# Kernel tuning notes

Hardware: AMD Instinct MI355X
Metric: run time of the kernel (lower is better)

The kernel has to match this reference:

```python
import jax, jax.numpy as jnp
import numpy as np

PATCH = 3          # patch size for SSD cost
PAD = PATCH // 2
K_NN = 8           # number of NN candidates kept per pixel
N_ITERS = 10       # PatchMatch iterations (forward default n_iters=10)
_DY = jnp.array([d // PATCH for d in range(PATCH * PATCH)], dtype=jnp.int32)
_DX = jnp.array([d % PATCH for d in range(PATCH * PATCH)], dtype=jnp.int32)


def _patches(x):
    # x: [C,H,W] -> [C, P*P, H, W] edge-padded patch neighborhoods
    C, H, W = x.shape
    xp = jnp.pad(x, ((0, 0), (PAD, PAD), (PAD, PAD)), mode='edge')
    return jnp.stack([xp[:, dy:dy + H, dx:dx + W]
                      for dy in range(PATCH) for dx in range(PATCH)], axis=1)


def _cost(a_pat, b_pad, s):
    # a_pat: [C,P2,H,W]; b_pad: [C,H+2p,W+2p]; s: [2,H,W] int -> SSD cost [H,W]
    iy = s[0][None] + _DY[:, None, None]   # [P2,H,W]
    ix = s[1][None] + _DX[:, None, None]
    b_g = b_pad[:, iy, ix]                 # [C,P2,H,W] gathered target patches
    return jnp.sum((a_pat - b_g) ** 2, axis=(0, 1))


def patchmatch_search(a, b, key, k=K_NN, n_iters=N_ITERS):
    # a, b: [C,H,W]. Returns shifts [k,2,H,W] int32 and costs [k,H,W].
    C, H, W = a.shape
    a_pat = _patches(a)
    b_pad = jnp.pad(b, ((0, 0), (PAD, PAD), (PAD, PAD)), mode='edge')
    cost1 = lambda s: _cost(a_pat, b_pad, s)
    hi = jnp.array([H, W], dtype=jnp.int32).reshape(1, 2, 1, 1)
    dx1 = jnp.array([0, 1], jnp.int32).reshape(1, 2, 1, 1)
    dy1 = jnp.array([1, 0], jnp.int32).reshape(1, 2, 1, 1)
    k0, key = jax.random.split(key)
    shifts = jax.random.randint(k0, (k, 2, H, W), 0, hi)
    costs = jax.lax.map(cost1, shifts)
    radii = [max(W // 2, 1), max(W // 8, 1), max(W // 32, 1), 1]

    def step(carry, it):
        shifts, costs = carry
        kk = jax.random.fold_in(key, it)
        # parallel propagation of neighbors' shifts
        left = jnp.roll(shifts, 1, axis=3) + dx1
        right = jnp.roll(shifts, -1, axis=3) - dx1
        up = jnp.roll(shifts, 1, axis=2) + dy1
        down = jnp.roll(shifts, -1, axis=2) - dy1
        # random search with shrinking radii
        rand_c = [shifts + jax.random.randint(jax.random.fold_in(kk, i),
                                              shifts.shape, -r, r + 1)
                  for i, r in enumerate(radii)]
        cands = jnp.concatenate([left, right, up, down] + rand_c, axis=0)
        cands = jnp.clip(cands, 0, hi - 1)
        new_costs = jax.lax.map(cost1, cands)
        all_s = jnp.concatenate([shifts, cands], axis=0)      # [M,2,H,W]
        all_c = jnp.concatenate([costs, new_costs], axis=0)   # [M,H,W]
        neg_top, idx = jax.lax.top_k(-jnp.moveaxis(all_c, 0, -1), k)  # [H,W,k]
        s_hw = jnp.transpose(all_s, (2, 3, 0, 1))             # [H,W,M,2]
        sel = jnp.take_along_axis(s_hw, idx[..., None], axis=2)  # [H,W,k,2]
        return (jnp.transpose(sel, (2, 3, 0, 1)), jnp.moveaxis(-neg_top, -1, 0)), None

    (shifts, costs), _ = jax.lax.scan(step, (shifts, costs), jnp.arange(n_iters))
    return shifts, costs


def setup_inputs() -> dict:
    key = jax.random.key(0)
    kq, kk, kv = jax.random.split(key, 3)
    q = jax.random.normal(kq, (1, 32, 128, 128), jnp.float32)
    k = jax.random.normal(kk, (1, 32, 128, 128), jnp.float32)
    v = jax.random.normal(kv, (4, 64, 128, 128), jnp.float32)
    return {"q": q, "k": k, "v": v}


def reference(q, k, v):
    # PatchMatch k-NN search between q[0] and k[0]
    shifts, costs = patchmatch_search(q[0], k[0], jax.random.key(42))
    w = jax.nn.softmax(-costs, axis=0)                 # [K,H,W]
    g = v[:, :, shifts[:, 0], shifts[:, 1]]            # [B,Cv,K,H,W] gather
    return jnp.sum(w[None, None] * g, axis=2)          # [B,Cv,H,W]
```

## Files before the change

kernel.cpp:

```cpp
#include <hip/hip_runtime.h>
#include <cstdint>

#define NPIX 16384
#define KNN 8
#define PW 130
#define NPPAD (PW * PW)
#define NPH 8

typedef float f32x4 __attribute__((ext_vector_type(4)));
typedef __attribute__((address_space(3))) uint32_t lds_u32_t;
typedef const __attribute__((address_space(1))) uint32_t glob_u32_t;

__host__ __device__ __forceinline__ void tf2x32(uint32_t k0, uint32_t k1,
                                                uint32_t x0, uint32_t x1,
                                                uint32_t& o0, uint32_t& o1) {
  uint32_t ks2 = k0 ^ k1 ^ 0x1BD11BDAu;
  x0 += k0; x1 += k1;
#define TFR(r) { x0 += x1; x1 = (x1 << r) | (x1 >> (32 - r)); x1 ^= x0; }
  TFR(13) TFR(15) TFR(26) TFR(6)  x0 += k1;  x1 += ks2 + 1u;
  TFR(17) TFR(29) TFR(16) TFR(24) x0 += ks2; x1 += k0 + 2u;
  TFR(13) TFR(15) TFR(26) TFR(6)  x0 += k0;  x1 += k1 + 3u;
  TFR(17) TFR(29) TFR(16) TFR(24) x0 += k1;  x1 += ks2 + 4u;
  TFR(13) TFR(15) TFR(26) TFR(6)  x0 += ks2; x1 += k0 + 5u;
#undef TFR
  o0 = x0; o1 = x1;
}

__device__ __forceinline__ uint32_t rbits32(uint32_t ka, uint32_t kb, uint32_t j) {
  uint32_t o0, o1;
  tf2x32(ka, kb, 0u, j, o0, o1);
  return o0 ^ o1;
}

__device__ __forceinline__ int rnd_int(uint4 K, uint32_t j, uint32_t span,
                                       uint32_t mult, int minv) {
  uint32_t hi = rbits32(K.x, K.y, j);
  uint32_t lo = rbits32(K.z, K.w, j);
  uint32_t off = ((hi % span) * mult + (lo % span)) % span;
  return minv + (int)off;
}

__device__ __forceinline__ float cost_eval_pl(const float* __restrict__ apt,
                                              const float* __restrict__ bpt,
                                              int py0, int px0, int sy, int sx) {
  float acc = 0.f;
#pragma unroll
  for (int ph = 0; ph < NPH; ++ph) {
    const float* ab = apt + ((size_t)ph * NPPAD + (size_t)(py0 * PW + px0)) * 4;
    const float* bb = bpt + ((size_t)ph * NPPAD + (size_t)(sy * PW + sx)) * 4;
    f32x4 av[9], bv[9];
#pragma unroll
    for (int p = 0; p < 9; ++p) {
      int dy = p / 3, dx = p - dy * 3;
      av[p] = *(const f32x4*)(ab + (dy * PW + dx) * 4);
      bv[p] = *(const f32x4*)(bb + (dy * PW + dx) * 4);
    }
#pragma unroll
    for (int j = 0; j < 4; ++j) {
#pragma unroll
      for (int p = 0; p < 9; ++p) {
        float d = __fsub_rn(av[p][j], bv[p][j]);
        acc = __fadd_rn(acc, __fmul_rn(d, d));
      }
    }
  }
  return acc;
}

__global__ __launch_bounds__(256) void pad_kernel(
    const float* __restrict__ a, const float* __restrict__ b,
    float* __restrict__ apt, float* __restrict__ bpt) {
  int t = (int)(blockIdx.x * blockDim.x + threadIdx.x);
  if (t >= 32 * NPPAD) return;
  int lo = t & 3;
  int rest = t >> 2;
  int pos = rest % NPPAD;
  int ph = rest / NPPAD;
  int c = ph * 4 + lo;
  int py = pos / PW, px = pos % PW;
  int y = py - 1; y = y < 0 ? 0 : (y > 127 ? 127 : y);
  int x = px - 1; x = x < 0 ? 0 : (x > 127 ? 127 : x);
  int src = (c << 14) + (y << 7) + x;
  apt[t] = a[src];
  bpt[t] = b[src];
}

__global__ __launch_bounds__(256) void init_kernel(
    const float* __restrict__ apt, const float* __restrict__ bpt,
    uint32_t* __restrict__ npack, float* __restrict__ ncost, uint4 IK) {
  int t = (int)(blockIdx.x * blockDim.x + threadIdx.x);
  int pix = t & (NPIX - 1);
  int s = t >> 14;
  int py0 = pix >> 7, px0 = pix & 127;
  uint32_t j0 = (uint32_t)(s * 2) * 16384u + (uint32_t)pix;
  int sy = rnd_int(IK, j0, 128u, 0u, 0);
  int sx = rnd_int(IK, j0 + 16384u, 128u, 0u, 0);
  float cst = cost_eval_pl(apt, bpt, py0, px0, sy, sx);
  npack[t] = (uint32_t)((sy << 7) | sx);
  ncost[t] = cst;
}

__global__ __launch_bounds__(64, 4) void step_kernel(
    const float* __restrict__ apt, const float* __restrict__ bpt,
    const uint32_t* __restrict__ ppack, const float* __restrict__ pcost,
    uint32_t* __restrict__ npack, float* __restrict__ ncost,
    uint4 K0, uint4 K1, uint4 K2, uint4 K3) {
  __shared__ f32x4 ldsb[576];
  __shared__ f32x4 ldsa[72];
  int bidx = (int)blockIdx.x;
  int pix = ((bidx & 7) << 11) | (bidx >> 3);
  int lane = (int)threadIdx.x;
  int py0 = pix >> 7, px0 = pix & 127;
  int g = lane >> 3, s = lane & 7;

  uint32_t old_pack = 0u; float old_cost_f = 0.f;
  if (lane < 8) {
    old_pack = ppack[lane * NPIX + pix];
    old_cost_f = pcost[lane * NPIX + pix];
  }

  int sy, sx;
  if (g < 4) {
    int nh = py0, nw = px0, dsy = 0, dsx = 0;
    if (g == 0)      { nw = (px0 + 127) & 127; dsx = 1;  }
    else if (g == 1) { nw = (px0 + 1) & 127;   dsx = -1; }
    else if (g == 2) { nh = (py0 + 127) & 127; dsy = 1;  }
    else             { nh = (py0 + 1) & 127;   dsy = -1; }
    uint32_t p = ppack[s * NPIX + (nh << 7) + nw];
    sy = (int)(p >> 7) + dsy;
    sx = (int)(p & 127u) + dsx;
  } else {
    uint32_t p = ppack[s * NPIX + pix];
    uint4 Ki      = (g == 4) ? K0   : (g == 5) ? K1  : (g == 6) ? K2 : K3;
    uint32_t span = (g == 4) ? 129u : (g == 5) ? 33u : (g == 6) ? 9u : 3u;
    uint32_t mult = (g == 4) ? 16u  : (g == 5) ? 4u  : (g == 6) ? 4u : 1u;
    int minv      = (g == 4) ? -64  : (g == 5) ? -16 : (g == 6) ? -4 : -1;
    uint32_t j0 = (uint32_t)(s * 2) * 16384u + (uint32_t)pix;
    sy = (int)(p >> 7)   + rnd_int(Ki, j0, span, mult, minv);
    sx = (int)(p & 127u) + rnd_int(Ki, j0 + 16384u, span, mult, minv);
  }
  sy = sy < 0 ? 0 : (sy > 127 ? 127 : sy);
  sx = sx < 0 ? 0 : (sx > 127 ? 127 : sx);
  uint32_t cnd_pack = (uint32_t)((sy << 7) | sx);

  int base_[9];
#pragma unroll
  for (int i = 0; i < 9; ++i) {
    int f = i * 64 + lane;
    int c = f / 9, p = f - c * 9;
    int dy = p / 3, dx = p - dy * 3;
    uint32_t pk = (uint32_t)__shfl((int)cnd_pack, c);
    int py = (int)(pk >> 7) + dy;
    int px = (int)(pk & 127u) + dx;
    base_[i] = (py * PW + px) * 4;
  }

  {
    int q = lane;
    int ph = q / 9, pos = q - ph * 9;
    int dy = pos / 3, dx = pos - dy * 3;
    const float* gp = apt + (size_t)ph * (NPPAD * 4)
                     + (size_t)((py0 + dy) * PW + (px0 + dx)) * 4;
    __builtin_amdgcn_global_load_lds((glob_u32_t*)gp, (lds_u32_t*)&ldsa[0], 16, 0, 0);
  }
  if (lane < 8) {
    int q = 64 + lane;
    int ph = q / 9, pos = q - ph * 9;
    int dy = pos / 3, dx = pos - dy * 3;
    const float* gp = apt + (size_t)ph * (NPPAD * 4)
                     + (size_t)((py0 + dy) * PW + (px0 + dx)) * 4;
    __builtin_amdgcn_global_load_lds((glob_u32_t*)gp, (lds_u32_t*)&ldsa[64], 16, 0, 0);
  }

#define GLB(PH)                                                             \
  _Pragma("unroll")                                                         \
  for (int i = 0; i < 9; ++i) {                                             \
    __builtin_amdgcn_global_load_lds(                                       \
        (glob_u32_t*)(bpt + (size_t)(PH) * (NPPAD * 4) + base_[i]),         \
        (lds_u32_t*)&ldsb[i * 64], 16, 0, 0);                               \
  }

  GLB(0)

  float acc = 0.f;

#define PHASE(PH, DOGL)                                                     \
  asm volatile("s_waitcnt vmcnt(0)" ::: "memory");                          \
  {                                                                         \
    f32x4 av[9], bv[9];                                                     \
    _Pragma("unroll")                                                       \
    for (int p = 0; p < 9; ++p) {                                           \
      bv[p] = ldsb[lane * 9 + p];                                           \
      av[p] = ldsa[(PH) * 9 + p];                                           \
    }                                                                       \
    asm volatile("s_waitcnt lgkmcnt(0)" ::: "memory");                      \
    DOGL                                                                    \
    _Pragma("unroll")                                                       \
    for (int j = 0; j < 4; ++j) {                                           \
      _Pragma("unroll")                                                     \
      for (int p = 0; p < 9; ++p) {                                         \
        float d = __fsub_rn(av[p][j], bv[p][j]);                            \
        acc = __fadd_rn(acc, __fmul_rn(d, d));                              \
      }                                                                     \
    }                                                                       \
  }

  PHASE(0, GLB(1))
  PHASE(1, GLB(2))
  PHASE(2, GLB(3))
  PHASE(3, GLB(4))
  PHASE(4, GLB(5))
  PHASE(5, GLB(6))
  PHASE(6, GLB(7))
  PHASE(7, )
#undef PHASE
#undef GLB

  float cnd_cost = acc;

  unsigned long long new_key =
      ((unsigned long long)__float_as_uint(cnd_cost) << 32) | (unsigned)(8 + lane);
  unsigned long long old_key = (lane < 8)
      ? (((unsigned long long)__float_as_uint(old_cost_f) << 32) | (unsigned)lane)
      : ~0ull;
  bool new_used = false, old_used = (lane >= 8);

  uint32_t out_pack = 0u; float out_cost = 0.f;
#define TOPK_ROUND(R)                                                      \
  {                                                                        \
    unsigned long long kmin = new_used ? ~0ull : new_key;                  \
    if (!old_used && old_key < kmin) kmin = old_key;                       \
    _Pragma("unroll")                                                      \
    for (int off = 32; off; off >>= 1) {                                   \
      unsigned long long o = __shfl_xor(kmin, off);                        \
      if (o < kmin) kmin = o;                                              \
    }                                                                      \
    if (!new_used && new_key == kmin) new_used = true;                     \
    else if (!old_used && old_key == kmin) old_used = true;                \
    uint32_t idx = (uint32_t)kmin;                                         \
    float cst = __uint_as_float((uint32_t)(kmin >> 32));                   \
    int srcOld = (idx < 8u) ? (int)idx : 0;                                \
    int srcNew = (idx >= 8u) ? (int)(idx - 8u) : 0;                        \
    uint32_t po = __shfl(old_pack, srcOld);                                \
    uint32_t pn = __shfl(cnd_pack, srcNew);                                \
    uint32_t pk = (idx < 8u) ? po : pn;                                    \
    if (lane == R) { out_pack = pk; out_cost = cst; }                      \
  }
  TOPK_ROUND(0) TOPK_ROUND(1) TOPK_ROUND(2) TOPK_ROUND(3)
  TOPK_ROUND(4) TOPK_ROUND(5) TOPK_ROUND(6) TOPK_ROUND(7)
#undef TOPK_ROUND

  if (lane < 8) {
    npack[lane * NPIX + pix] = out_pack;
    ncost[lane * NPIX + pix] = out_cost;
  }
}

__global__ __launch_bounds__(256) void weights_kernel(
    const float* __restrict__ cost0, float* __restrict__ wbuf) {
  int pix = (int)(blockIdx.x * blockDim.x + threadIdx.x);
  if (pix >= NPIX) return;
  float c[KNN];
  float m = 3.4e38f;
#pragma unroll
  for (int s = 0; s < KNN; ++s) { c[s] = cost0[s * NPIX + pix]; m = fminf(m, c[s]); }
  float e[KNN]; float sum = 0.f;
#pragma unroll
  for (int s = 0; s < KNN; ++s) { e[s] = expf(m - c[s]); sum += e[s]; }
  float inv = 1.f / sum;
#pragma unroll
  for (int s = 0; s < KNN; ++s) wbuf[s * NPIX + pix] = e[s] * inv;
}

__global__ __launch_bounds__(256) void out_kernel(
    const float* __restrict__ v, const uint32_t* __restrict__ pack0,
    const float* __restrict__ wbuf, float* __restrict__ out) {
  int t = (int)(blockIdx.x * blockDim.x + threadIdx.x);
  int pix = t & (NPIX - 1);
  int ch = t >> 14;
  const float* vc = v + ((size_t)ch << 14);
  float acc = 0.f;
#pragma unroll
  for (int s = 0; s < KNN; ++s) {
    uint32_t p = pack0[s * NPIX + pix];
    float wgt = wbuf[s * NPIX + pix];
    acc = fmaf(wgt, vc[p], acc);
  }
  out[t] = acc;
}

static void h_split_fl(uint32_t ka, uint32_t kb, uint32_t o[4]) {
  tf2x32(ka, kb, 0u, 0u, o[0], o[1]);
  tf2x32(ka, kb, 0u, 1u, o[2], o[3]);
}

extern "C" void kernel_launch(void* const* d_in, const int* in_sizes, int n_in,
                              void* d_out, int out_size, void* d_ws, size_t ws_size,
                              hipStream_t stream) {
  const float* q = (const float*)d_in[0];
  const float* k = (const float*)d_in[1];
  const float* v = (const float*)d_in[2];
  float* out = (float*)d_out;

  uint32_t* ws = (uint32_t*)d_ws;
  uint32_t* pk[2] = { ws, ws + (size_t)KNN * NPIX };
  float* ct[2] = { (float*)(ws + (size_t)2 * KNN * NPIX),
                   (float*)(ws + (size_t)3 * KNN * NPIX) };
  float* wbuf = (float*)(ws + (size_t)4 * KNN * NPIX);
  float* apt  = (float*)(ws + (size_t)5 * KNN * NPIX);
  float* bpt  = apt + (size_t)32 * NPPAD;

  uint32_t sp[4];
  h_split_fl(0u, 42u, sp);
  uint32_t k0a = sp[0], k0b = sp[1];
  uint32_t kMa = sp[2], kMb = sp[3];

  pad_kernel<<<(32 * NPPAD + 255) / 256, 256, 0, stream>>>(q, k, apt, bpt);

  uint32_t ik[4];
  h_split_fl(k0a, k0b, ik);
  init_kernel<<<(KNN * NPIX) / 256, 256, 0, stream>>>(apt, bpt, pk[0], ct[0],
                                        make_uint4(ik[0], ik[1], ik[2], ik[3]));

  for (int it = 0; it < 10; ++it) {
    uint32_t ka, kb;
    tf2x32(kMa, kMb, 0u, (uint32_t)it, ka, kb);
    uint4 K[4];
    for (int i = 0; i < 4; ++i) {
      uint32_t ia, ib;
      tf2x32(ka, kb, 0u, (uint32_t)i, ia, ib);
      uint32_t o[4];
      h_split_fl(ia, ib, o);
      K[i] = make_uint4(o[0], o[1], o[2], o[3]);
    }
    step_kernel<<<NPIX, 64, 0, stream>>>(apt, bpt, pk[it & 1], ct[it & 1],
                                         pk[(it + 1) & 1], ct[(it + 1) & 1],
                                         K[0], K[1], K[2], K[3]);
  }

  weights_kernel<<<NPIX / 256, 256, 0, stream>>>(ct[0], wbuf);
  out_kernel<<<(4 * 64 * NPIX) / 256, 256, 0, stream>>>(v, pk[0], wbuf, out);
}
```

Baseline: 906.2 us.

## Regroup padded planes into 16-channel pixels and stage target patches in two phases

The padded feature planes change from 8 groups of 4 channels to 2 groups of 16 channels per pixel, so each 3x3 patch read covers wider contiguous chunks. The step kernel now stages candidate patches into LDS in 2 phases of 37 loads per lane instead of 8 phases of 9. Query-side values are read straight from global memory instead of through an LDS copy. This cuts per-phase wait and barrier overhead, but raises LDS use per block and the number of address computations and shuffles per phase.

```diff
diff --git a/kernel.cpp b/kernel.cpp
--- a/kernel.cpp
+++ b/kernel.cpp
@@ -5,7 +5,8 @@
 #define KNN 8
 #define PW 130
 #define NPPAD (PW * PW)
-#define NPH 8
+#define PLANE (NPPAD * 16)
+#define QC 37
 
 typedef float f32x4 __attribute__((ext_vector_type(4)));
 typedef __attribute__((address_space(3))) uint32_t lds_u32_t;
@@ -45,22 +46,25 @@
                                               int py0, int px0, int sy, int sx) {
   float acc = 0.f;
 #pragma unroll
-  for (int ph = 0; ph < NPH; ++ph) {
-    const float* ab = apt + ((size_t)ph * NPPAD + (size_t)(py0 * PW + px0)) * 4;
-    const float* bb = bpt + ((size_t)ph * NPPAD + (size_t)(sy * PW + sx)) * 4;
-    f32x4 av[9], bv[9];
-#pragma unroll
-    for (int p = 0; p < 9; ++p) {
-      int dy = p / 3, dx = p - dy * 3;
-      av[p] = *(const f32x4*)(ab + (dy * PW + dx) * 4);
-      bv[p] = *(const f32x4*)(bb + (dy * PW + dx) * 4);
-    }
-#pragma unroll
-    for (int j = 0; j < 4; ++j) {
+  for (int hh = 0; hh < 2; ++hh) {
+    const float* ab = apt + (size_t)hh * PLANE + (size_t)(py0 * PW + px0) * 16;
+    const float* bb = bpt + (size_t)hh * PLANE + (size_t)(sy * PW + sx) * 16;
+#pragma unroll
+    for (int cc = 0; cc < 4; ++cc) {
+      f32x4 av[9], bv[9];
 #pragma unroll
       for (int p = 0; p < 9; ++p) {
-        float d = __fsub_rn(av[p][j], bv[p][j]);
-        acc = __fadd_rn(acc, __fmul_rn(d, d));
+        int dy = p / 3, dx = p - dy * 3;
+        av[p] = *(const f32x4*)(ab + (dy * PW + dx) * 16 + cc * 4);
+        bv[p] = *(const f32x4*)(bb + (dy * PW + dx) * 16 + cc * 4);
+      }
+#pragma unroll
+      for (int j = 0; j < 4; ++j) {
+#pragma unroll
+        for (int p = 0; p < 9; ++p) {
+          float d = __fsub_rn(av[p][j], bv[p][j]);
+          acc = __fadd_rn(acc, __fmul_rn(d, d));
+        }
       }
     }
   }
@@ -72,11 +76,11 @@
     float* __restrict__ apt, float* __restrict__ bpt) {
   int t = (int)(blockIdx.x * blockDim.x + threadIdx.x);
   if (t >= 32 * NPPAD) return;
-  int lo = t & 3;
-  int rest = t >> 2;
+  int lo = t & 15;
+  int rest = t >> 4;
   int pos = rest % NPPAD;
-  int ph = rest / NPPAD;
-  int c = ph * 4 + lo;
+  int hh = rest / NPPAD;
+  int c = hh * 16 + lo;
   int py = pos / PW, px = pos % PW;
   int y = py - 1; y = y < 0 ? 0 : (y > 127 ? 127 : y);
   int x = px - 1; x = x < 0 ? 0 : (x > 127 ? 127 : x);
@@ -105,8 +109,7 @@
     const uint32_t* __restrict__ ppack, const float* __restrict__ pcost,
     uint32_t* __restrict__ npack, float* __restrict__ ncost,
     uint4 K0, uint4 K1, uint4 K2, uint4 K3) {
-  __shared__ f32x4 ldsb[576];
-  __shared__ f32x4 ldsa[72];
+  __shared__ f32x4 ldsb[64 * QC];
   int bidx = (int)blockIdx.x;
   int pix = ((bidx & 7) << 11) | (bidx >> 3);
   int lane = (int)threadIdx.x;
@@ -143,40 +146,21 @@
   sx = sx < 0 ? 0 : (sx > 127 ? 127 : sx);
   uint32_t cnd_pack = (uint32_t)((sy << 7) | sx);
 
-  int base_[9];
-#pragma unroll
-  for (int i = 0; i < 9; ++i) {
-    int f = i * 64 + lane;
-    int c = f / 9, p = f - c * 9;
-    int dy = p / 3, dx = p - dy * 3;
-    uint32_t pk = (uint32_t)__shfl((int)cnd_pack, c);
-    int py = (int)(pk >> 7) + dy;
-    int px = (int)(pk & 127u) + dx;
-    base_[i] = (py * PW + px) * 4;
-  }
-
-  {
-    int q = lane;
-    int ph = q / 9, pos = q - ph * 9;
-    int dy = pos / 3, dx = pos - dy * 3;
-    const float* gp = apt + (size_t)ph * (NPPAD * 4)
-                     + (size_t)((py0 + dy) * PW + (px0 + dx)) * 4;
-    __builtin_amdgcn_global_load_lds((glob_u32_t*)gp, (lds_u32_t*)&ldsa[0], 16, 0, 0);
-  }
-  if (lane < 8) {
-    int q = 64 + lane;
-    int ph = q / 9, pos = q - ph * 9;
-    int dy = pos / 3, dx = pos - dy * 3;
-    const float* gp = apt + (size_t)ph * (NPPAD * 4)
-                     + (size_t)((py0 + dy) * PW + (px0 + dx)) * 4;
-    __builtin_amdgcn_global_load_lds((glob_u32_t*)gp, (lds_u32_t*)&ldsa[64], 16, 0, 0);
-  }
-
 #define GLB(PH)                                                             \
   _Pragma("unroll")                                                         \
-  for (int i = 0; i < 9; ++i) {                                             \
+  for (int i = 0; i < QC; ++i) {                                            \
+    int f = i * 64 + lane;                                                  \
+    int c = f / QC, q = f - c * QC;                                         \
+    uint32_t pk = (uint32_t)__shfl((int)cnd_pack, c);                       \
+    int off = 0;                                                            \
+    if (q < 36) {                                                           \
+      int p = q >> 2, cc = q & 3;                                           \
+      int dy = p / 3, dx = p - dy * 3;                                      \
+      off = (((int)(pk >> 7) + dy) * PW + (int)(pk & 127u) + dx) * 16       \
+            + cc * 4;                                                       \
+    }                                                                       \
     __builtin_amdgcn_global_load_lds(                                       \
-        (glob_u32_t*)(bpt + (size_t)(PH) * (NPPAD * 4) + base_[i]),         \
+        (glob_u32_t*)(bpt + (size_t)(PH) * PLANE + off),                    \
         (lds_u32_t*)&ldsb[i * 64], 16, 0, 0);                               \
   }
 
@@ -184,35 +168,37 @@
 
   float acc = 0.f;
 
-#define PHASE(PH, DOGL)                                                     \
+#define PHASE(HH, DO_NEXT)                                                  \
   asm volatile("s_waitcnt vmcnt(0)" ::: "memory");                          \
   {                                                                         \
-    f32x4 av[9], bv[9];                                                     \
+    const float* ab = apt + (size_t)(HH) * PLANE                            \
+                     + (size_t)(py0 * PW + px0) * 16;                       \
     _Pragma("unroll")                                                       \
-    for (int p = 0; p < 9; ++p) {                                           \
-      bv[p] = ldsb[lane * 9 + p];                                           \
-      av[p] = ldsa[(PH) * 9 + p];                                           \
-    }                                                                       \
-    asm volatile("s_waitcnt lgkmcnt(0)" ::: "memory");                      \
-    DOGL                                                                    \
-    _Pragma("unroll")                                                       \
-    for (int j = 0; j < 4; ++j) {                                           \
+    for (int cc = 0; cc < 4; ++cc) {                                        \
+      f32x4 av[9], bv[9];                                                   \
       _Pragma("unroll")                                                     \
       for (int p = 0; p < 9; ++p) {                                         \
-        float d = __fsub_rn(av[p][j], bv[p][j]);                            \
-        acc = __fadd_rn(acc, __fmul_rn(d, d));                              \
+        int dy = p / 3, dx = p - dy * 3;                                    \
+        bv[p] = ldsb[lane * QC + p * 4 + cc];                               \
+        av[p] = *(const f32x4*)(ab + (dy * PW + dx) * 16 + cc * 4);         \
+      }                                                                     \
+      if (cc == 3) {                                                        \
+        asm volatile("s_waitcnt lgkmcnt(0)" ::: "memory");                  \
+        DO_NEXT                                                             \
+      }                                                                     \
+      _Pragma("unroll")                                                     \
+      for (int j = 0; j < 4; ++j) {                                         \
+        _Pragma("unroll")                                                   \
+        for (int p = 0; p < 9; ++p) {                                       \
+          float d = __fsub_rn(av[p][j], bv[p][j]);                          \
+          acc = __fadd_rn(acc, __fmul_rn(d, d));                            \
+        }                                                                   \
       }                                                                     \
     }                                                                       \
   }
 
   PHASE(0, GLB(1))
-  PHASE(1, GLB(2))
-  PHASE(2, GLB(3))
-  PHASE(3, GLB(4))
-  PHASE(4, GLB(5))
-  PHASE(5, GLB(6))
-  PHASE(6, GLB(7))
-  PHASE(7, )
+  PHASE(1, )
 #undef PHASE
 #undef GLB
 
```

Result: slower. 2.053 ms (+126.6%).

## Restructure init cost via LDS staging; fuse softmax-gather with transposed v

Applied to the files above, without the earlier changes.

The init kernel now uses 64-thread blocks covering 8 pixels times 8 candidates, staging gathered target patches into LDS with async global-to-LDS loads that are pipelined across channel phases, mirroring the step kernel. A new transpose kernel lays v out pixel-major with 256 channels contiguous. A fused output kernel then computes the softmax weights and performs a coalesced weighted gather per pixel, replacing the separate weights and strided-gather kernels. This adds an extra transpose pass and workspace memory, and falls back to the old path if the workspace is too small.

```diff
diff --git a/kernel.cpp b/kernel.cpp
--- a/kernel.cpp
+++ b/kernel.cpp
@@ -38,33 +38,6 @@
   uint32_t lo = rbits32(K.z, K.w, j);
   uint32_t off = ((hi % span) * mult + (lo % span)) % span;
   return minv + (int)off;
-}
-
-__device__ __forceinline__ float cost_eval_pl(const float* __restrict__ apt,
-                                              const float* __restrict__ bpt,
-                                              int py0, int px0, int sy, int sx) {
-  float acc = 0.f;
-#pragma unroll
-  for (int ph = 0; ph < NPH; ++ph) {
-    const float* ab = apt + ((size_t)ph * NPPAD + (size_t)(py0 * PW + px0)) * 4;
-    const float* bb = bpt + ((size_t)ph * NPPAD + (size_t)(sy * PW + sx)) * 4;
-    f32x4 av[9], bv[9];
-#pragma unroll
-    for (int p = 0; p < 9; ++p) {
-      int dy = p / 3, dx = p - dy * 3;
-      av[p] = *(const f32x4*)(ab + (dy * PW + dx) * 4);
-      bv[p] = *(const f32x4*)(bb + (dy * PW + dx) * 4);
-    }
-#pragma unroll
-    for (int j = 0; j < 4; ++j) {
-#pragma unroll
-      for (int p = 0; p < 9; ++p) {
-        float d = __fsub_rn(av[p][j], bv[p][j]);
-        acc = __fadd_rn(acc, __fmul_rn(d, d));
-      }
-    }
-  }
-  return acc;
 }
 
 __global__ __launch_bounds__(256) void pad_kernel(
@@ -85,19 +58,87 @@
   bpt[t] = b[src];
 }
 
-__global__ __launch_bounds__(256) void init_kernel(
+__global__ __launch_bounds__(256) void vtr_kernel(
+    const float* __restrict__ v, float* __restrict__ vtr) {
+  int t = (int)(blockIdx.x * blockDim.x + threadIdx.x);
+  int ch = t >> 14, pix = t & (NPIX - 1);
+  vtr[(size_t)pix * 256 + ch] = v[t];
+}
+
+__global__ __launch_bounds__(64, 4) void init_kernel(
     const float* __restrict__ apt, const float* __restrict__ bpt,
     uint32_t* __restrict__ npack, float* __restrict__ ncost, uint4 IK) {
-  int t = (int)(blockIdx.x * blockDim.x + threadIdx.x);
-  int pix = t & (NPIX - 1);
-  int s = t >> 14;
+  __shared__ f32x4 ldsb[576];
+  int bidx = (int)blockIdx.x;
+  int gid = (bidx & 7) * 256 + (bidx >> 3);
+  int lane = (int)threadIdx.x;
+  int s = lane >> 3, pp = lane & 7;
+  int pix = gid * 8 + pp;
   int py0 = pix >> 7, px0 = pix & 127;
   uint32_t j0 = (uint32_t)(s * 2) * 16384u + (uint32_t)pix;
   int sy = rnd_int(IK, j0, 128u, 0u, 0);
   int sx = rnd_int(IK, j0 + 16384u, 128u, 0u, 0);
-  float cst = cost_eval_pl(apt, bpt, py0, px0, sy, sx);
-  npack[t] = (uint32_t)((sy << 7) | sx);
-  ncost[t] = cst;
+  uint32_t cnd_pack = (uint32_t)((sy << 7) | sx);
+
+  int base_[9];
+#pragma unroll
+  for (int i = 0; i < 9; ++i) {
+    int f = i * 64 + lane;
+    int c = f / 9, p = f - c * 9;
+    int dy = p / 3, dx = p - dy * 3;
+    uint32_t pk = (uint32_t)__shfl((int)cnd_pack, c);
+    int py = (int)(pk >> 7) + dy;
+    int px = (int)(pk & 127u) + dx;
+    base_[i] = (py * PW + px) * 4;
+  }
+
+#define GLBI(PH)                                                            \
+  _Pragma("unroll")                                                         \
+  for (int i = 0; i < 9; ++i) {                                             \
+    __builtin_amdgcn_global_load_lds(                                       \
+        (glob_u32_t*)(bpt + (size_t)(PH) * (NPPAD * 4) + base_[i]),         \
+        (lds_u32_t*)&ldsb[i * 64], 16, 0, 0);                               \
+  }
+
+  GLBI(0)
+
+  float acc = 0.f;
+#define IPHASE(PH, DOGL)                                                    \
+  asm volatile("s_waitcnt vmcnt(0)" ::: "memory");                          \
+  {                                                                         \
+    f32x4 av[9], bv[9];                                                     \
+    _Pragma("unroll")                                                       \
+    for (int p = 0; p < 9; ++p) {                                           \
+      int dy = p / 3, dx = p - dy * 3;                                      \
+      bv[p] = ldsb[lane * 9 + p];                                           \
+      av[p] = *(const f32x4*)(apt + (size_t)(PH) * (NPPAD * 4)              \
+              + (size_t)((py0 + dy) * PW + (px0 + dx)) * 4);                \
+    }                                                                       \
+    asm volatile("s_waitcnt lgkmcnt(0)" ::: "memory");                      \
+    DOGL                                                                    \
+    _Pragma("unroll")                                                       \
+    for (int j = 0; j < 4; ++j) {                                           \
+      _Pragma("unroll")                                                     \
+      for (int p = 0; p < 9; ++p) {                                         \
+        float d = __fsub_rn(av[p][j], bv[p][j]);                            \
+        acc = __fadd_rn(acc, __fmul_rn(d, d));                              \
+      }                                                                     \
+    }                                                                       \
+  }
+
+  IPHASE(0, GLBI(1))
+  IPHASE(1, GLBI(2))
+  IPHASE(2, GLBI(3))
+  IPHASE(3, GLBI(4))
+  IPHASE(4, GLBI(5))
+  IPHASE(5, GLBI(6))
+  IPHASE(6, GLBI(7))
+  IPHASE(7, )
+#undef IPHASE
+#undef GLBI
+
+  npack[s * NPIX + pix] = cnd_pack;
+  ncost[s * NPIX + pix] = acc;
 }
 
 __global__ __launch_bounds__(64, 4) void step_kernel(
@@ -183,7 +224,6 @@
   GLB(0)
 
   float acc = 0.f;
-
 #define PHASE(PH, DOGL)                                                     \
   asm volatile("s_waitcnt vmcnt(0)" ::: "memory");                          \
   {                                                                         \
@@ -256,6 +296,43 @@
   }
 }
 
+__global__ __launch_bounds__(64) void outfused_kernel(
+    const float* __restrict__ vtr, const uint32_t* __restrict__ pack0,
+    const float* __restrict__ cost0, float* __restrict__ out) {
+  int bidx = (int)blockIdx.x;
+  int pix = ((bidx & 7) << 11) | (bidx >> 3);
+  int lane = (int)threadIdx.x;
+  float cv = 0.f; uint32_t pv = 0u;
+  if (lane < 8) {
+    cv = cost0[lane * NPIX + pix];
+    pv = pack0[lane * NPIX + pix];
+  }
+  float c[KNN]; uint32_t p[KNN];
+#pragma unroll
+  for (int s = 0; s < KNN; ++s) {
+    c[s] = __shfl(cv, s);
+    p[s] = (uint32_t)__shfl((int)pv, s);
+  }
+  float m = c[0];
+#pragma unroll
+  for (int s = 1; s < KNN; ++s) m = fminf(m, c[s]);
+  float e[KNN]; float sum = 0.f;
+#pragma unroll
+  for (int s = 0; s < KNN; ++s) { e[s] = expf(m - c[s]); sum += e[s]; }
+  float inv = 1.f / sum;
+  f32x4 acc = {0.f, 0.f, 0.f, 0.f};
+#pragma unroll
+  for (int s = 0; s < KNN; ++s) {
+    f32x4 r = *(const f32x4*)(vtr + (size_t)p[s] * 256 + lane * 4);
+    float w = e[s] * inv;
+#pragma unroll
+    for (int j = 0; j < 4; ++j) acc[j] = fmaf(w, r[j], acc[j]);
+  }
+#pragma unroll
+  for (int j = 0; j < 4; ++j)
+    out[(size_t)(lane * 4 + j) * NPIX + pix] = acc[j];
+}
+
 __global__ __launch_bounds__(256) void weights_kernel(
     const float* __restrict__ cost0, float* __restrict__ wbuf) {
   int pix = (int)(blockIdx.x * blockDim.x + threadIdx.x);
@@ -309,6 +386,10 @@
   float* wbuf = (float*)(ws + (size_t)4 * KNN * NPIX);
   float* apt  = (float*)(ws + (size_t)5 * KNN * NPIX);
   float* bpt  = apt + (size_t)32 * NPPAD;
+  float* vtr  = bpt + (size_t)32 * NPPAD;
+  size_t need = ((size_t)5 * KNN * NPIX + (size_t)64 * NPPAD
+                 + (size_t)4 * 64 * NPIX) * 4u;
+  bool use_vtr = (ws_size >= need);
 
   uint32_t sp[4];
   h_split_fl(0u, 42u, sp);
@@ -316,10 +397,12 @@
   uint32_t kMa = sp[2], kMb = sp[3];
 
   pad_kernel<<<(32 * NPPAD + 255) / 256, 256, 0, stream>>>(q, k, apt, bpt);
+  if (use_vtr)
+    vtr_kernel<<<(4 * 64 * NPIX) / 256, 256, 0, stream>>>(v, vtr);
 
   uint32_t ik[4];
   h_split_fl(k0a, k0b, ik);
-  init_kernel<<<(KNN * NPIX) / 256, 256, 0, stream>>>(apt, bpt, pk[0], ct[0],
+  init_kernel<<<NPIX / 8, 64, 0, stream>>>(apt, bpt, pk[0], ct[0],
                                         make_uint4(ik[0], ik[1], ik[2], ik[3]));
 
   for (int it = 0; it < 10; ++it) {
@@ -338,6 +421,10 @@
                                          K[0], K[1], K[2], K[3]);
   }
 
-  weights_kernel<<<NPIX / 256, 256, 0, stream>>>(ct[0], wbuf);
-  out_kernel<<<(4 * 64 * NPIX) / 256, 256, 0, stream>>>(v, pk[0], wbuf, out);
-}
+  if (use_vtr) {
+    outfused_kernel<<<NPIX, 64, 0, stream>>>(vtr, pk[0], ct[0], out);
+  } else {
+    weights_kernel<<<NPIX / 256, 256, 0, stream>>>(ct[0], wbuf);
+    out_kernel<<<(4 * 64 * NPIX) / 256, 256, 0, stream>>>(v, pk[0], wbuf, out);
+  }
+}
```

Result: no change. 891.7 us (-1.6%).
